# Kernel optimization log

Measured on AMD Instinct MI355X. Metric: run time of the kernel, lower is better.

## Reference

```python
import jax, jax.numpy as jnp
import numpy as np

N_NODES = 50000
N_EDGES = 800000
N_FEAT = 128
HIDDEN = 128
HEADS = 4
C = HIDDEN // HEADS  # per-head channels = 32
N_LAYERS = 3
OUT_DIM = 2048
N_GRAPHS = 1000
LEAKY = 0.2  # PyG GATConv default negative_slope


def setup_inputs() -> dict:
    key = jax.random.key(0)
    ks = jax.random.split(key, 12)
    x = jax.random.normal(ks[0], (N_NODES, N_FEAT), dtype=jnp.float32)
    edge_index = jax.random.randint(ks[1], (2, N_EDGES), 0, N_NODES, dtype=jnp.int32)
    edge_attr = jax.random.normal(ks[2], (N_EDGES, 1), dtype=jnp.float32)
    batch = (jnp.arange(N_NODES, dtype=jnp.int32) // (N_NODES // N_GRAPHS))  # 50 nodes per graph
    s = 1.0 / np.sqrt(HIDDEN)
    Ws = jax.random.normal(ks[3], (N_LAYERS, N_FEAT, HIDDEN), dtype=jnp.float32) * s
    att_src = jax.random.normal(ks[4], (N_LAYERS, HEADS, C), dtype=jnp.float32) * s
    att_dst = jax.random.normal(ks[5], (N_LAYERS, HEADS, C), dtype=jnp.float32) * s
    We = jax.random.normal(ks[6], (N_LAYERS, 1, HIDDEN), dtype=jnp.float32) * s
    att_e = jax.random.normal(ks[7], (N_LAYERS, HEADS, C), dtype=jnp.float32) * s
    biases = jnp.zeros((N_LAYERS, HIDDEN), dtype=jnp.float32)
    lin1_w = jax.random.normal(ks[8], (HIDDEN, OUT_DIM), dtype=jnp.float32) * s
    lin1_b = jnp.zeros((OUT_DIM,), dtype=jnp.float32)
    return {"x": x, "edge_index": edge_index, "edge_attr": edge_attr, "batch": batch,
            "Ws": Ws, "att_src": att_src, "att_dst": att_dst, "We": We,
            "att_e": att_e, "biases": biases, "lin1_w": lin1_w, "lin1_b": lin1_b}


def _gat_layer(x, src, dst, ea, W, a_s, a_d, We_l, a_e, b):
    """PyG GATConv: shared lin for src/dst, edge_dim=1, concat heads, eval mode."""
    N = x.shape[0]
    h = (x @ W).reshape(N, HEADS, C)                       # [N,H,C]
    al_s = jnp.einsum('nhc,hc->nh', h, a_s)                # [N,H]
    al_d = jnp.einsum('nhc,hc->nh', h, a_d)
    e = (ea @ We_l).reshape(-1, HEADS, C)                  # [E',H,C]
    al_e = jnp.einsum('ehc,hc->eh', e, a_e)
    logits = jax.nn.leaky_relu(al_s[src] + al_d[dst] + al_e, LEAKY)  # [E',H]
    # segment softmax over incoming edges of each dst node, per head
    m = jax.ops.segment_max(logits, dst, num_segments=N)
    m = jnp.where(jnp.isfinite(m), m, 0.0)
    ex = jnp.exp(logits - m[dst])
    den = jax.ops.segment_sum(ex, dst, num_segments=N)
    alpha = ex / (den[dst] + 1e-16)                        # [E',H]
    msg = alpha[:, :, None] * h[src]                       # [E',H,C]
    out = jax.ops.segment_sum(msg, dst, num_segments=N)    # [N,H,C]
    return out.reshape(N, HIDDEN) + b


def reference(x, edge_index, edge_attr, batch, Ws, att_src, att_dst, We, att_e, biases, lin1_w, lin1_b):
    N = x.shape[0]
    src, dst = edge_index[0], edge_index[1]
    # add_self_loops=True with fill_value='mean' (PyG default): self-loop
    # edge_attr at node i = mean of edge_attr over edges pointing to i.
    cnt = jax.ops.segment_sum(jnp.ones_like(edge_attr[:, 0]), dst, num_segments=N)
    ea_sum = jax.ops.segment_sum(edge_attr, dst, num_segments=N)
    ea_self = jnp.where(cnt[:, None] > 0, ea_sum / jnp.maximum(cnt[:, None], 1.0), 0.0)
    loop = jnp.arange(N, dtype=src.dtype)
    src_f = jnp.concatenate([src, loop])
    dst_f = jnp.concatenate([dst, loop])
    ea_f = jnp.concatenate([edge_attr, ea_self], axis=0)
    for l in range(N_LAYERS):
        x = _gat_layer(x, src_f, dst_f, ea_f, Ws[l], att_src[l], att_dst[l], We[l], att_e[l], biases[l])
        x = jax.nn.relu(x)  # dropout is identity in eval mode
    pooled = jax.ops.segment_max(x, batch, num_segments=N_GRAPHS, indices_are_sorted=True)
    out = pooled @ lin1_w + lin1_b
    return jax.nn.sigmoid(out)  # classes_is_bit=True
```

## Files before the change

kernel.cpp:

```cpp
#include <hip/hip_runtime.h>
#include <hip/hip_bf16.h>
#include <math.h>

#define NN 50000
#define NE 800000
#define HID 128
#define HEADS 4
#define CH 32
#define NG 1000
#define OUTD 2048
#define LEAKY 0.2f
#define NB196 ((NN + 255) / 256)

typedef __attribute__((ext_vector_type(8))) short bshort8;
typedef __attribute__((ext_vector_type(4))) float floatx4;

__device__ __forceinline__ float lrelu(float v) { return fmaxf(v, LEAKY * v); }

__device__ __forceinline__ unsigned short f2bf(float f) {
    __hip_bfloat16 b = __float2bfloat16(f);
    return *reinterpret_cast<unsigned short*>(&b);
}
__device__ __forceinline__ float bflo(unsigned u) { return __uint_as_float(u << 16); }
__device__ __forceinline__ float bfhi(unsigned u) { return __uint_as_float(u & 0xffff0000u); }
__device__ __forceinline__ float bfu(unsigned short u) { return __uint_as_float(((unsigned)u) << 16); }

__global__ void k_hist(const int* __restrict__ ei, int* __restrict__ deg,
                       int* __restrict__ pos) {
    int e = blockIdx.x * 256 + threadIdx.x;
    if (e >= NE) return;
    pos[e] = atomicAdd(&deg[ei[NE + e]], 1);
}

__global__ __launch_bounds__(256) void k_s1(const int* __restrict__ deg,
                                            int* __restrict__ loc,
                                            int* __restrict__ bsum) {
    __shared__ int ws[4];
    int t = blockIdx.x * 256 + threadIdx.x;
    int lane = threadIdx.x & 63, wid = threadIdx.x >> 6;
    int v = (t < NN) ? deg[t] : 0;
    int run = v;
    for (int off = 1; off < 64; off <<= 1) {
        int u = __shfl_up(run, off);
        if (lane >= off) run += u;
    }
    if (lane == 63) ws[wid] = run;
    __syncthreads();
    int wadd = 0;
    if (wid > 0) wadd += ws[0];
    if (wid > 1) wadd += ws[1];
    if (wid > 2) wadd += ws[2];
    if (t < NN) loc[t] = run - v + wadd;
    if (threadIdx.x == 255) bsum[blockIdx.x] = wadd + run;
}

__global__ __launch_bounds__(256) void k_s2(const int* __restrict__ bsum,
                                            int* __restrict__ bexcl) {
    __shared__ int ws[4];
    int t = threadIdx.x;
    int lane = t & 63, wid = t >> 6;
    int v = (t < NB196) ? bsum[t] : 0;
    int run = v;
    for (int off = 1; off < 64; off <<= 1) {
        int u = __shfl_up(run, off);
        if (lane >= off) run += u;
    }
    if (lane == 63) ws[wid] = run;
    __syncthreads();
    int wadd = 0;
    if (wid > 0) wadd += ws[0];
    if (wid > 1) wadd += ws[1];
    if (wid > 2) wadd += ws[2];
    if (t < NB196) bexcl[t] = run - v + wadd;
}

__global__ __launch_bounds__(256) void k_s3(const int* __restrict__ loc,
                                            const int* __restrict__ bexcl,
                                            int* __restrict__ rowptr) {
    int t = blockIdx.x * 256 + threadIdx.x;
    if (t < NN) rowptr[t] = loc[t] + bexcl[blockIdx.x];
    if (t == 0) rowptr[NN] = NE;
}

__global__ void k_scatter(const int* __restrict__ ei, const float* __restrict__ ea,
                          const int* __restrict__ rowptr, const int* __restrict__ pos,
                          unsigned* __restrict__ ep) {
    int e = blockIdx.x * 256 + threadIdx.x;
    if (e >= NE) return;
    int d = ei[NE + e];
    unsigned rec = (((unsigned)f2bf(ea[e])) << 16) | (unsigned)ei[e];
    ep[rowptr[d] + pos[e]] = rec;
}

__global__ void k_coef(const float* __restrict__ We, const float* __restrict__ att_e,
                       float* __restrict__ coef) {
    int t = threadIdx.x;
    if (t < 12) {
        int l = t >> 2, hh = t & 3;
        const float* w = We + l * HID + hh * CH;
        const float* a = att_e + l * HID + hh * CH;
        float s = 0.f;
        for (int c = 0; c < CH; ++c) s += w[c] * a[c];
        coef[t] = s;
    }
}

__global__ void k_xcvt(const float* __restrict__ X, unsigned short* __restrict__ Xb) {
    int t = blockIdx.x * 256 + threadIdx.x;
    if (t >= NN * HID / 4) return;
    float4 v = ((const float4*)X)[t];
    ushort4 o;
    o.x = f2bf(v.x); o.y = f2bf(v.y); o.z = f2bf(v.z); o.w = f2bf(v.w);
    ((ushort4*)Xb)[t] = o;
}

__global__ void k_wt(const float* __restrict__ Ws, unsigned short* __restrict__ Wt) {
    int t = blockIdx.x * 256 + threadIdx.x;
    if (t >= 3 * HID * HID) return;
    int l = t / (HID * HID), rem = t % (HID * HID);
    int k = rem >> 7, n = rem & 127;
    Wt[l * HID * HID + n * HID + k] = f2bf(Ws[l * HID * HID + k * HID + n]);
}

__global__ __launch_bounds__(256) void k_mm(const unsigned short* __restrict__ Xb,
                                            const unsigned short* __restrict__ Wt,
                                            const float* __restrict__ aw_s,
                                            const float* __restrict__ aw_d,
                                            unsigned short* __restrict__ H2,
                                            float* __restrict__ als,
                                            float* __restrict__ ald) {
    int t = threadIdx.x;
    int wv = t >> 6, lane = t & 63;
    int m0 = blockIdx.x * 64 + wv * 16;
    int ln = lane & 15, kg = lane >> 4;
    int row = m0 + ln;
    int rc = row < NN ? row : NN - 1;
    floatx4 acc[8];
    #pragma unroll
    for (int nt = 0; nt < 8; ++nt) acc[nt] = (floatx4){0.f, 0.f, 0.f, 0.f};
    #pragma unroll
    for (int kc = 0; kc < HID; kc += 32) {
        bshort8 a = *(const bshort8*)&Xb[rc * HID + kc + kg * 8];
        #pragma unroll
        for (int nt = 0; nt < 8; ++nt) {
            bshort8 b = *(const bshort8*)&Wt[(nt * 16 + ln) * HID + kc + kg * 8];
            acc[nt] = __builtin_amdgcn_mfma_f32_16x16x32_bf16(a, b, acc[nt], 0, 0, 0);
        }
    }
    #pragma unroll
    for (int nt = 0; nt < 8; ++nt) {
        #pragma unroll
        for (int r = 0; r < 4; ++r) {
            int ro = m0 + kg * 4 + r;
            if (ro < NN) H2[ro * HID + nt * 16 + ln] = f2bf(acc[nt][r]);
        }
    }
    float ws8[8], wd8[8];
    #pragma unroll
    for (int nt = 0; nt < 8; ++nt) {
        ws8[nt] = aw_s[nt * 16 + ln];
        wd8[nt] = aw_d[nt * 16 + ln];
    }
    float pas[4][4], pad[4][4];
    #pragma unroll
    for (int h = 0; h < 4; ++h) {
        #pragma unroll
        for (int r = 0; r < 4; ++r) {
            pas[h][r] = acc[2 * h][r] * ws8[2 * h] + acc[2 * h + 1][r] * ws8[2 * h + 1];
            pad[h][r] = acc[2 * h][r] * wd8[2 * h] + acc[2 * h + 1][r] * wd8[2 * h + 1];
        }
    }
    #pragma unroll
    for (int h = 0; h < 4; ++h) {
        #pragma unroll
        for (int r = 0; r < 4; ++r) {
            #pragma unroll
            for (int off = 1; off < 16; off <<= 1) {
                pas[h][r] += __shfl_xor(pas[h][r], off);
                pad[h][r] += __shfl_xor(pad[h][r], off);
            }
        }
    }
    if (ln < 4) {
        #pragma unroll
        for (int r = 0; r < 4; ++r) {
            int ro = m0 + kg * 4 + r;
            if (ro < NN) {
                float vs = ln == 0 ? pas[0][r] : ln == 1 ? pas[1][r]
                         : ln == 2 ? pas[2][r] : pas[3][r];
                float vd = ln == 0 ? pad[0][r] : ln == 1 ? pad[1][r]
                         : ln == 2 ? pad[2][r] : pad[3][r];
                als[ro * 4 + ln] = vs;
                ald[ro * 4 + ln] = vd;
            }
        }
    }
}

__global__ __launch_bounds__(256) void k_agg(const int* __restrict__ rowptr,
                                             const unsigned* __restrict__ ep,
                                             const float* __restrict__ als,
                                             const float* __restrict__ ald,
                                             const unsigned short* __restrict__ H2,
                                             const float* __restrict__ coef_l,
                                             const float* __restrict__ bias,
                                             unsigned short* __restrict__ xout) {
    int n = blockIdx.x * 4 + (threadIdx.x >> 6);
    int lane = threadIdx.x & 63;
    int slot = lane >> 4, lpos = lane & 15;
    int hh = lpos >> 2;
    int ch0 = lpos * 8;
    const uint4* H2q = (const uint4*)H2;
    float coefh = coef_l[hh];
    float aldh = ald[n * 4 + hh];
    float s = 0.f, ea = 0.f;
    float acc[8];
    #pragma unroll
    for (int i = 0; i < 8; ++i) acc[i] = 0.f;
    int jb = rowptr[n], je = rowptr[n + 1];
    for (int j = jb; j < je; j += 8) {
        int eA = j + slot;
        bool vA = eA < je;
        unsigned recA = vA ? ep[eA] : 0u;
        int srcA = vA ? (int)(recA & 0xffffu) : n;
        float aA = bfhi(recA);
        uint4 hA = H2q[srcA * 16 + lpos];
        float pA = vA ? __expf(lrelu(als[srcA * 4 + hh] + aldh + aA * coefh)) : 0.f;
        int eB = j + 4 + slot;
        bool vB = eB < je;
        unsigned recB = vB ? ep[eB] : 0u;
        int srcB = vB ? (int)(recB & 0xffffu) : n;
        float aB = bfhi(recB);
        uint4 hB = H2q[srcB * 16 + lpos];
        float pB = vB ? __expf(lrelu(als[srcB * 4 + hh] + aldh + aB * coefh)) : 0.f;
        s += pA + pB;
        ea += aA + aB;
        acc[0] += pA * bflo(hA.x) + pB * bflo(hB.x);
        acc[1] += pA * bfhi(hA.x) + pB * bfhi(hB.x);
        acc[2] += pA * bflo(hA.y) + pB * bflo(hB.y);
        acc[3] += pA * bfhi(hA.y) + pB * bfhi(hB.y);
        acc[4] += pA * bflo(hA.z) + pB * bflo(hB.z);
        acc[5] += pA * bfhi(hA.z) + pB * bfhi(hB.z);
        acc[6] += pA * bflo(hA.w) + pB * bflo(hB.w);
        acc[7] += pA * bfhi(hA.w) + pB * bfhi(hB.w);
    }
    #pragma unroll
    for (int i = 0; i < 8; ++i) {
        acc[i] += __shfl_xor(acc[i], 16);
        acc[i] += __shfl_xor(acc[i], 32);
    }
    s += __shfl_xor(s, 16);  s += __shfl_xor(s, 32);
    ea += __shfl_xor(ea, 16); ea += __shfl_xor(ea, 32);
    int degn = je - jb;
    float eaself = (degn > 0) ? ea / (float)degn : 0.f;
    float ps = __expf(lrelu(als[n * 4 + hh] + aldh + eaself * coefh));
    uint4 hv = H2q[n * 16 + lpos];
    s += ps;
    acc[0] += ps * bflo(hv.x);
    acc[1] += ps * bfhi(hv.x);
    acc[2] += ps * bflo(hv.y);
    acc[3] += ps * bfhi(hv.y);
    acc[4] += ps * bflo(hv.z);
    acc[5] += ps * bfhi(hv.z);
    acc[6] += ps * bflo(hv.w);
    acc[7] += ps * bfhi(hv.w);
    float inv = 1.0f / (s + 1e-16f);
    if (slot == 0) {
        float4 b0 = *(const float4*)&bias[ch0];
        float4 b1 = *(const float4*)&bias[ch0 + 4];
        float o0 = fmaxf(acc[0] * inv + b0.x, 0.f);
        float o1 = fmaxf(acc[1] * inv + b0.y, 0.f);
        float o2 = fmaxf(acc[2] * inv + b0.z, 0.f);
        float o3 = fmaxf(acc[3] * inv + b0.w, 0.f);
        float o4 = fmaxf(acc[4] * inv + b1.x, 0.f);
        float o5 = fmaxf(acc[5] * inv + b1.y, 0.f);
        float o6 = fmaxf(acc[6] * inv + b1.z, 0.f);
        float o7 = fmaxf(acc[7] * inv + b1.w, 0.f);
        uint4 ov;
        ov.x = (((unsigned)f2bf(o1)) << 16) | f2bf(o0);
        ov.y = (((unsigned)f2bf(o3)) << 16) | f2bf(o2);
        ov.z = (((unsigned)f2bf(o5)) << 16) | f2bf(o4);
        ov.w = (((unsigned)f2bf(o7)) << 16) | f2bf(o6);
        *(uint4*)&xout[n * HID + ch0] = ov;
    }
}

__global__ void k_pool(const unsigned short* __restrict__ x, float* __restrict__ pooled) {
    int g = blockIdx.x;
    int c = threadIdx.x;
    float m = -INFINITY;
    const unsigned short* p = x + g * 50 * HID + c;
    for (int i = 0; i < 50; ++i) m = fmaxf(m, bfu(p[i * HID]));
    pooled[g * HID + c] = m;
}

__global__ __launch_bounds__(256) void k_out(const float* __restrict__ pooled,
                                             const float* __restrict__ W,
                                             const float* __restrict__ b,
                                             float* __restrict__ out) {
    __shared__ float sp[8][HID];
    int t = threadIdx.x;
    int o = blockIdx.x * 256 + t;
    int g0 = blockIdx.y * 8;
    for (int i = t; i < 8 * HID / 4; i += 256)
        ((float4*)sp)[i] = ((const float4*)(pooled + g0 * HID))[i];
    __syncthreads();
    float acc[8];
    #pragma unroll
    for (int g = 0; g < 8; ++g) acc[g] = 0.f;
    for (int k = 0; k < HID; ++k) {
        float wv = W[k * OUTD + o];
        #pragma unroll
        for (int g = 0; g < 8; ++g) acc[g] += sp[g][k] * wv;
    }
    float bb = b[o];
    #pragma unroll
    for (int g = 0; g < 8; ++g)
        out[(g0 + g) * OUTD + o] = 1.f / (1.f + expf(-(acc[g] + bb)));
}

extern "C" void kernel_launch(void* const* d_in, const int* in_sizes, int n_in,
                              void* d_out, int out_size, void* d_ws, size_t ws_size,
                              hipStream_t stream) {
    const float* x_in    = (const float*)d_in[0];
    const int*   ei      = (const int*)d_in[1];
    const float* ea      = (const float*)d_in[2];
    const float* Ws      = (const float*)d_in[4];
    const float* att_src = (const float*)d_in[5];
    const float* att_dst = (const float*)d_in[6];
    const float* We      = (const float*)d_in[7];
    const float* att_e   = (const float*)d_in[8];
    const float* biases  = (const float*)d_in[9];
    const float* lin1_w  = (const float*)d_in[10];
    const float* lin1_b  = (const float*)d_in[11];
    float* out = (float*)d_out;

    char* p = (char*)d_ws;
    int*   deg    = (int*)p;                 p += sizeof(int) * NN;
    int*   loc    = (int*)p;                 p += sizeof(int) * NN;
    int*   bsum   = (int*)p;                 p += sizeof(int) * 256;
    int*   bexcl  = (int*)p;                 p += sizeof(int) * 256;
    int*   rowptr = (int*)p;                 p += sizeof(int) * (NN + 1);
    p += sizeof(int) * 3;
    int*   pos    = (int*)p;                 p += sizeof(int) * NE;
    unsigned* ep  = (unsigned*)p;            p += sizeof(unsigned) * (NE + 8);
    unsigned short* H2  = (unsigned short*)p; p += sizeof(short) * (size_t)NN * HID;
    unsigned short* Xb0 = (unsigned short*)p; p += sizeof(short) * (size_t)NN * HID;
    unsigned short* xa  = (unsigned short*)p; p += sizeof(short) * (size_t)NN * HID;
    unsigned short* xb  = (unsigned short*)p; p += sizeof(short) * (size_t)NN * HID;
    unsigned short* Wt  = (unsigned short*)p; p += sizeof(short) * 3 * HID * HID;
    float* als    = (float*)p;               p += sizeof(float) * NN * HEADS;
    float* ald    = (float*)p;               p += sizeof(float) * NN * HEADS;
    float* pooled = (float*)p;               p += sizeof(float) * NG * HID;
    float* coef   = (float*)p;               p += sizeof(float) * 12;

    hipMemsetAsync(deg, 0, sizeof(int) * NN, stream);
    k_hist<<<(NE + 255) / 256, 256, 0, stream>>>(ei, deg, pos);
    k_s1<<<NB196, 256, 0, stream>>>(deg, loc, bsum);
    k_s2<<<1, 256, 0, stream>>>(bsum, bexcl);
    k_s3<<<NB196, 256, 0, stream>>>(loc, bexcl, rowptr);
    k_scatter<<<(NE + 255) / 256, 256, 0, stream>>>(ei, ea, rowptr, pos, ep);
    k_coef<<<1, 64, 0, stream>>>(We, att_e, coef);
    k_wt<<<(3 * HID * HID + 255) / 256, 256, 0, stream>>>(Ws, Wt);
    k_xcvt<<<(NN * HID / 4 + 255) / 256, 256, 0, stream>>>(x_in, Xb0);

    for (int l = 0; l < 3; ++l) {
        const unsigned short* xin = (l == 0) ? Xb0 : (l == 1 ? xa : xb);
        unsigned short* xout      = (l == 1) ? xb : xa;
        k_mm<<<(NN + 63) / 64, 256, 0, stream>>>(xin, Wt + l * HID * HID,
                                                 att_src + l * HEADS * CH,
                                                 att_dst + l * HEADS * CH,
                                                 H2, als, ald);
        k_agg<<<NN / 4, 256, 0, stream>>>(rowptr, ep, als, ald,
                                          H2, coef + l * 4, biases + l * HID, xout);
    }
    k_pool<<<NG, HID, 0, stream>>>(xa, pooled);
    dim3 og(OUTD / 256, NG / 8);
    k_out<<<og, 256, 0, stream>>>(pooled, lin1_w, lin1_b, out);
}
```

Measured before the change: 411.6 us.

## Fuse setup kernels, merge scan stages, unroll aggregation loop to 16 edges

Setup work (x bf16 conversion, weight transpose, degree zeroing, edge coefficients) is merged into one kernel, replacing a memset and three launches. The second and third scan kernels are combined so that each block reduces the preceding block sums itself. The aggregation loop now handles 16 edges per iteration instead of 8, putting more independent gathers in flight. The intent is to cut launch overhead and hide gather latency, at the cost of redundant per-block reductions and higher register pressure in the aggregation kernel.

```diff
diff --git a/kernel.cpp b/kernel.cpp
--- a/kernel.cpp
+++ b/kernel.cpp
@@ -24,6 +24,37 @@
 __device__ __forceinline__ float bflo(unsigned u) { return __uint_as_float(u << 16); }
 __device__ __forceinline__ float bfhi(unsigned u) { return __uint_as_float(u & 0xffff0000u); }
 __device__ __forceinline__ float bfu(unsigned short u) { return __uint_as_float(((unsigned)u) << 16); }
+
+__global__ __launch_bounds__(256) void k_setup(const float* __restrict__ X,
+                                               unsigned short* __restrict__ Xb,
+                                               const float* __restrict__ Ws,
+                                               unsigned short* __restrict__ Wt,
+                                               const float* __restrict__ We,
+                                               const float* __restrict__ att_e,
+                                               float* __restrict__ coef,
+                                               int* __restrict__ deg) {
+    int tid = blockIdx.x * 256 + threadIdx.x;
+    if (tid < NN * HID / 4) {
+        float4 v = ((const float4*)X)[tid];
+        ushort4 o;
+        o.x = f2bf(v.x); o.y = f2bf(v.y); o.z = f2bf(v.z); o.w = f2bf(v.w);
+        ((ushort4*)Xb)[tid] = o;
+    }
+    if (tid < 3 * HID * HID) {
+        int l = tid / (HID * HID), rem = tid % (HID * HID);
+        int k = rem >> 7, n = rem & 127;
+        Wt[l * HID * HID + n * HID + k] = f2bf(Ws[l * HID * HID + k * HID + n]);
+    }
+    if (tid < NN / 4) ((int4*)deg)[tid] = make_int4(0, 0, 0, 0);
+    if (tid < 12) {
+        int l = tid >> 2, hh = tid & 3;
+        const float* w = We + l * HID + hh * CH;
+        const float* a = att_e + l * HID + hh * CH;
+        float s = 0.f;
+        for (int c = 0; c < CH; ++c) s += w[c] * a[c];
+        coef[tid] = s;
+    }
+}
 
 __global__ void k_hist(const int* __restrict__ ei, int* __restrict__ deg,
                        int* __restrict__ pos) {
@@ -54,32 +85,21 @@
     if (threadIdx.x == 255) bsum[blockIdx.x] = wadd + run;
 }
 
-__global__ __launch_bounds__(256) void k_s2(const int* __restrict__ bsum,
-                                            int* __restrict__ bexcl) {
+__global__ __launch_bounds__(256) void k_s3(const int* __restrict__ loc,
+                                            const int* __restrict__ bsum,
+                                            int* __restrict__ rowptr) {
     __shared__ int ws[4];
-    int t = threadIdx.x;
-    int lane = t & 63, wid = t >> 6;
-    int v = (t < NB196) ? bsum[t] : 0;
-    int run = v;
-    for (int off = 1; off < 64; off <<= 1) {
-        int u = __shfl_up(run, off);
-        if (lane >= off) run += u;
-    }
-    if (lane == 63) ws[wid] = run;
+    int t = threadIdx.x, b = blockIdx.x;
+    int v = (t < b && t < NB196) ? bsum[t] : 0;
+    int r = v;
+    #pragma unroll
+    for (int off = 1; off < 64; off <<= 1) r += __shfl_xor(r, off);
+    if ((t & 63) == 0) ws[t >> 6] = r;
     __syncthreads();
-    int wadd = 0;
-    if (wid > 0) wadd += ws[0];
-    if (wid > 1) wadd += ws[1];
-    if (wid > 2) wadd += ws[2];
-    if (t < NB196) bexcl[t] = run - v + wadd;
-}
-
-__global__ __launch_bounds__(256) void k_s3(const int* __restrict__ loc,
-                                            const int* __restrict__ bexcl,
-                                            int* __restrict__ rowptr) {
-    int t = blockIdx.x * 256 + threadIdx.x;
-    if (t < NN) rowptr[t] = loc[t] + bexcl[blockIdx.x];
-    if (t == 0) rowptr[NN] = NE;
+    int bex = ws[0] + ws[1] + ws[2] + ws[3];
+    int g = b * 256 + t;
+    if (g < NN) rowptr[g] = loc[g] + bex;
+    if (g == 0) rowptr[NN] = NE;
 }
 
 __global__ void k_scatter(const int* __restrict__ ei, const float* __restrict__ ea,
@@ -90,36 +110,6 @@
     int d = ei[NE + e];
     unsigned rec = (((unsigned)f2bf(ea[e])) << 16) | (unsigned)ei[e];
     ep[rowptr[d] + pos[e]] = rec;
-}
-
-__global__ void k_coef(const float* __restrict__ We, const float* __restrict__ att_e,
-                       float* __restrict__ coef) {
-    int t = threadIdx.x;
-    if (t < 12) {
-        int l = t >> 2, hh = t & 3;
-        const float* w = We + l * HID + hh * CH;
-        const float* a = att_e + l * HID + hh * CH;
-        float s = 0.f;
-        for (int c = 0; c < CH; ++c) s += w[c] * a[c];
-        coef[t] = s;
-    }
-}
-
-__global__ void k_xcvt(const float* __restrict__ X, unsigned short* __restrict__ Xb) {
-    int t = blockIdx.x * 256 + threadIdx.x;
-    if (t >= NN * HID / 4) return;
-    float4 v = ((const float4*)X)[t];
-    ushort4 o;
-    o.x = f2bf(v.x); o.y = f2bf(v.y); o.z = f2bf(v.z); o.w = f2bf(v.w);
-    ((ushort4*)Xb)[t] = o;
-}
-
-__global__ void k_wt(const float* __restrict__ Ws, unsigned short* __restrict__ Wt) {
-    int t = blockIdx.x * 256 + threadIdx.x;
-    if (t >= 3 * HID * HID) return;
-    int l = t / (HID * HID), rem = t % (HID * HID);
-    int k = rem >> 7, n = rem & 127;
-    Wt[l * HID * HID + n * HID + k] = f2bf(Ws[l * HID * HID + k * HID + n]);
 }
 
 __global__ __launch_bounds__(256) void k_mm(const unsigned short* __restrict__ Xb,
@@ -218,23 +208,29 @@
     #pragma unroll
     for (int i = 0; i < 8; ++i) acc[i] = 0.f;
     int jb = rowptr[n], je = rowptr[n + 1];
-    for (int j = jb; j < je; j += 8) {
-        int eA = j + slot;
-        bool vA = eA < je;
+    for (int j = jb; j < je; j += 16) {
+        int eA = j + slot,      eB = j + 4 + slot;
+        int eC = j + 8 + slot,  eD = j + 12 + slot;
+        bool vA = eA < je, vB = eB < je, vC = eC < je, vD = eD < je;
         unsigned recA = vA ? ep[eA] : 0u;
+        unsigned recB = vB ? ep[eB] : 0u;
+        unsigned recC = vC ? ep[eC] : 0u;
+        unsigned recD = vD ? ep[eD] : 0u;
         int srcA = vA ? (int)(recA & 0xffffu) : n;
-        float aA = bfhi(recA);
+        int srcB = vB ? (int)(recB & 0xffffu) : n;
+        int srcC = vC ? (int)(recC & 0xffffu) : n;
+        int srcD = vD ? (int)(recD & 0xffffu) : n;
         uint4 hA = H2q[srcA * 16 + lpos];
+        uint4 hB = H2q[srcB * 16 + lpos];
+        uint4 hC = H2q[srcC * 16 + lpos];
+        uint4 hD = H2q[srcD * 16 + lpos];
+        float aA = bfhi(recA), aB = bfhi(recB), aC = bfhi(recC), aD = bfhi(recD);
         float pA = vA ? __expf(lrelu(als[srcA * 4 + hh] + aldh + aA * coefh)) : 0.f;
-        int eB = j + 4 + slot;
-        bool vB = eB < je;
-        unsigned recB = vB ? ep[eB] : 0u;
-        int srcB = vB ? (int)(recB & 0xffffu) : n;
-        float aB = bfhi(recB);
-        uint4 hB = H2q[srcB * 16 + lpos];
         float pB = vB ? __expf(lrelu(als[srcB * 4 + hh] + aldh + aB * coefh)) : 0.f;
-        s += pA + pB;
-        ea += aA + aB;
+        float pC = vC ? __expf(lrelu(als[srcC * 4 + hh] + aldh + aC * coefh)) : 0.f;
+        float pD = vD ? __expf(lrelu(als[srcD * 4 + hh] + aldh + aD * coefh)) : 0.f;
+        s += (pA + pB) + (pC + pD);
+        ea += (aA + aB) + (aC + aD);
         acc[0] += pA * bflo(hA.x) + pB * bflo(hB.x);
         acc[1] += pA * bfhi(hA.x) + pB * bfhi(hB.x);
         acc[2] += pA * bflo(hA.y) + pB * bflo(hB.y);
@@ -243,6 +239,14 @@
         acc[5] += pA * bfhi(hA.z) + pB * bfhi(hB.z);
         acc[6] += pA * bflo(hA.w) + pB * bflo(hB.w);
         acc[7] += pA * bfhi(hA.w) + pB * bfhi(hB.w);
+        acc[0] += pC * bflo(hC.x) + pD * bflo(hD.x);
+        acc[1] += pC * bfhi(hC.x) + pD * bfhi(hD.x);
+        acc[2] += pC * bflo(hC.y) + pD * bflo(hD.y);
+        acc[3] += pC * bfhi(hC.y) + pD * bfhi(hD.y);
+        acc[4] += pC * bflo(hC.z) + pD * bflo(hD.z);
+        acc[5] += pC * bfhi(hC.z) + pD * bfhi(hD.z);
+        acc[6] += pC * bflo(hC.w) + pD * bflo(hD.w);
+        acc[7] += pC * bfhi(hC.w) + pD * bfhi(hD.w);
     }
     #pragma unroll
     for (int i = 0; i < 8; ++i) {
@@ -339,11 +343,10 @@
     int*   deg    = (int*)p;                 p += sizeof(int) * NN;
     int*   loc    = (int*)p;                 p += sizeof(int) * NN;
     int*   bsum   = (int*)p;                 p += sizeof(int) * 256;
-    int*   bexcl  = (int*)p;                 p += sizeof(int) * 256;
     int*   rowptr = (int*)p;                 p += sizeof(int) * (NN + 1);
     p += sizeof(int) * 3;
     int*   pos    = (int*)p;                 p += sizeof(int) * NE;
-    unsigned* ep  = (unsigned*)p;            p += sizeof(unsigned) * (NE + 8);
+    unsigned* ep  = (unsigned*)p;            p += sizeof(unsigned) * (NE + 16);
     unsigned short* H2  = (unsigned short*)p; p += sizeof(short) * (size_t)NN * HID;
     unsigned short* Xb0 = (unsigned short*)p; p += sizeof(short) * (size_t)NN * HID;
     unsigned short* xa  = (unsigned short*)p; p += sizeof(short) * (size_t)NN * HID;
@@ -354,15 +357,12 @@
     float* pooled = (float*)p;               p += sizeof(float) * NG * HID;
     float* coef   = (float*)p;               p += sizeof(float) * 12;
 
-    hipMemsetAsync(deg, 0, sizeof(int) * NN, stream);
+    k_setup<<<(NN * HID / 4 + 255) / 256, 256, 0, stream>>>(x_in, Xb0, Ws, Wt,
+                                                            We, att_e, coef, deg);
     k_hist<<<(NE + 255) / 256, 256, 0, stream>>>(ei, deg, pos);
     k_s1<<<NB196, 256, 0, stream>>>(deg, loc, bsum);
-    k_s2<<<1, 256, 0, stream>>>(bsum, bexcl);
-    k_s3<<<NB196, 256, 0, stream>>>(loc, bexcl, rowptr);
+    k_s3<<<NB196, 256, 0, stream>>>(loc, bsum, rowptr);
     k_scatter<<<(NE + 255) / 256, 256, 0, stream>>>(ei, ea, rowptr, pos, ep);
-    k_coef<<<1, 64, 0, stream>>>(We, att_e, coef);
-    k_wt<<<(3 * HID * HID + 255) / 256, 256, 0, stream>>>(Ws, Wt);
-    k_xcvt<<<(NN * HID / 4 + 255) / 256, 256, 0, stream>>>(x_in, Xb0);
 
     for (int l = 0; l < 3; ++l) {
         const unsigned short* xin = (l == 0) ? Xb0 : (l == 1 ? xa : xb);
```

Measured after the change: 399.6 us. 1.03x faster.
